# Kernel optimization log

Measured on AMD Instinct MI355X. Metric: run time of the kernel, lower is better.

The kernel has to match this reference:

```python
import jax, jax.numpy as jnp
import numpy as np

B, L, H = 4, 1024, 1024
NH, HD = 16, 64
ND = NH * HD
ITERS = 4
U = 5  # MSA1 ring window size (hard-coded in source)


def _conv1x1(w, b, x):  # w [O,C], b [O], x [B,C,L] -> [B,O,L]  (Conv2d 1x1 == per-position linear)
    return jnp.einsum('oc,bcl->bol', w, x) + b[None, :, None]


def _layernorm(x, s, b, eps=1e-5):  # x [B,H,L]; LayerNorm over channel dim H
    mu = x.mean(1, keepdims=True)
    var = ((x - mu) ** 2).mean(1, keepdims=True)
    return (x - mu) / jnp.sqrt(var + eps) * s[None, :, None] + b[None, :, None]


def _msa1(x, ax, wq, bq, wk, bk, wv, bv, wo, bo):
    # x [B,H,L] normalized nodes; ax [B,H,2,L] (ring embedding + relay)
    b, h, l = x.shape
    q = _conv1x1(wq, bq, x).reshape(b, NH, HD, l)
    k = _conv1x1(wk, bk, x).reshape(b, NH, HD, l)
    v = _conv1x1(wv, bv, x).reshape(b, NH, HD, l)
    pad = U // 2
    kp = jnp.pad(k, ((0, 0), (0, 0), (0, 0), (pad, pad)))
    vp = jnp.pad(v, ((0, 0), (0, 0), (0, 0), (pad, pad)))
    # F.unfold with (U,1) kernel along L == stack of U shifted views
    kw = jnp.stack([kp[..., u:u + l] for u in range(U)], axis=3)  # [B,NH,HD,U,L]
    vw = jnp.stack([vp[..., u:u + l] for u in range(U)], axis=3)
    al = ax.shape[2]
    ak = (jnp.einsum('oc,bcal->boal', wk, ax) + bk[None, :, None, None]).reshape(b, NH, HD, al, l)
    av = (jnp.einsum('oc,bcal->boal', wv, ax) + bv[None, :, None, None]).reshape(b, NH, HD, al, l)
    kw = jnp.concatenate([kw, ak], axis=3)  # [B,NH,HD,U+2,L]
    vw = jnp.concatenate([vw, av], axis=3)
    scores = (q[:, :, :, None, :] * kw).sum(2) / np.sqrt(HD)  # [B,NH,U+2,L]
    alphas = jax.nn.softmax(scores, axis=2)
    att = (alphas[:, :, None, :, :] * vw).sum(3).reshape(b, ND, l)
    return _conv1x1(wo, bo, att)  # [B,H,L]


def _msa2(relay, y, smask, wq, bq, wk, bk, wo, bo):
    # relay [B,H]; y [B,H,L+1]; smask [B,L+1] True at padding
    b = relay.shape[0]
    q = (jnp.einsum('oc,bc->bo', wq, relay) + bq).reshape(b, NH, HD)
    k = _conv1x1(wk, bk, y).reshape(b, NH, HD, -1)
    pre = jnp.einsum('bnd,bndl->bnl', q, k) / np.sqrt(HD)
    pre = jnp.where(smask[:, None, :], -1e10, pre)
    alphas = jax.nn.softmax(pre, axis=-1)
    # NOTE: source has v = k (WV output unused) -- reproduced faithfully
    att = jnp.einsum('bnl,bndl->bnd', alphas, k).reshape(b, ND)
    return jnp.einsum('oc,bc->bo', wo, att) + bo  # [B,H]


def _star_forward(data, mask, ln_s, ln_b, rwq, rwq_b, rwk, rwk_b, rwv, rwv_b, rwo, rwo_b,
                  swq, swq_b, swk, swk_b, swo, swo_b):
    b, l, h = data.shape
    pad_mask = (mask == 0)  # True at padding positions
    smask = jnp.concatenate([jnp.zeros((b, 1), bool), pad_mask], axis=1)  # [B,L+1]
    embs = jnp.transpose(data, (0, 2, 1))  # [B,H,L]
    nodes = embs
    relay = embs.mean(2)  # [B,H]
    for i in range(ITERS):
        xn = _layernorm(nodes, ln_s[i], ln_b[i])
        ax = jnp.stack([embs, jnp.broadcast_to(relay[:, :, None], embs.shape)], axis=2)  # [B,H,2,L]
        ring = _msa1(xn, ax, rwq[i], rwq_b[i], rwk[i], rwk_b[i], rwv[i], rwv_b[i], rwo[i], rwo_b[i])
        nodes = nodes + jax.nn.leaky_relu(ring)
        y = jnp.concatenate([relay[:, :, None], nodes], axis=2)  # [B,H,L+1]
        relay = jax.nn.leaky_relu(_msa2(relay, y, smask, swq[i], swq_b[i], swk[i], swk_b[i], swo[i], swo_b[i]))
        nodes = jnp.where(pad_mask[:, None, :], 0.0, nodes)
    return jnp.transpose(nodes, (0, 2, 1)), relay  # [B,L,H], [B,H]


def setup_inputs() -> dict:
    key = jax.random.key(0)
    ks = jax.random.split(key, 16)
    def p(k, shape):
        return jax.random.normal(k, shape, jnp.float32) * 0.02
    return dict(
        data=jax.random.normal(ks[0], (B, L, H), jnp.float32),
        mask=jax.random.randint(ks[1], (B, L), 0, 2).astype(jnp.int32),
        ln_s=jnp.ones((ITERS, H), jnp.float32),
        ln_b=jnp.zeros((ITERS, H), jnp.float32),
        rwq=p(ks[2], (ITERS, ND, H)), rwq_b=p(ks[3], (ITERS, ND)),
        rwk=p(ks[4], (ITERS, ND, H)), rwk_b=p(ks[5], (ITERS, ND)),
        rwv=p(ks[6], (ITERS, ND, H)), rwv_b=p(ks[7], (ITERS, ND)),
        rwo=p(ks[8], (ITERS, H, ND)), rwo_b=p(ks[9], (ITERS, H)),
        swq=p(ks[10], (ITERS, ND, H)), swq_b=p(ks[11], (ITERS, ND)),
        swk=p(ks[12], (ITERS, ND, H)), swk_b=p(ks[13], (ITERS, ND)),
        swo=p(ks[14], (ITERS, H, ND)), swo_b=p(ks[15], (ITERS, H)),
    )


def reference(data, mask, ln_s, ln_b, rwq, rwq_b, rwk, rwk_b, rwv, rwv_b, rwo, rwo_b,
              swq, swq_b, swk, swk_b, swo, swo_b):
    return _star_forward(data, mask, ln_s, ln_b, rwq, rwq_b, rwk, rwk_b, rwv, rwv_b,
                         rwo, rwo_b, swq, swq_b, swk, swk_b, swo, swo_b)
```

## Files before the change

### kernel.cpp

```cpp
#include <hip/hip_runtime.h>
#include <math.h>

namespace {

constexpr int B_ = 4, L_ = 1024, H_ = 1024, NH_ = 16, HD_ = 64, ND_ = 1024, ITERS_ = 4;

typedef unsigned short u16;
typedef __attribute__((ext_vector_type(8))) short short8;
typedef __attribute__((ext_vector_type(4))) float f32x4;

__device__ inline u16 f2bf(float f) {
  unsigned u = __builtin_bit_cast(unsigned, f);
  u += 0x7FFFu + ((u >> 16) & 1u);
  return (u16)(u >> 16);
}
__device__ inline float bf2f(u16 v) {
  unsigned u = ((unsigned)v) << 16;
  return __builtin_bit_cast(float, u);
}

__device__ inline void gl_lds16(const u16* g, u16* l) {
  __builtin_amdgcn_global_load_lds((const __attribute__((address_space(1))) void*)g,
                                   (__attribute__((address_space(3))) void*)l, 16, 0, 0);
}

__global__ void k_prep(const float* __restrict__ data, const float* __restrict__ rwq,
                       const float* __restrict__ rwk, const float* __restrict__ rwv,
                       const float* __restrict__ rwo, const float* __restrict__ swk,
                       u16* __restrict__ embs_bf, u16* __restrict__ wq_bf,
                       u16* __restrict__ wk_bf, u16* __restrict__ wv_bf,
                       u16* __restrict__ wo_bf, u16* __restrict__ swk_bf,
                       float* __restrict__ nodes) {
  int i = blockIdx.x * 256 + threadIdx.x;
  int which = blockIdx.y;
  if (which == 6) {
    reinterpret_cast<float4*>(nodes)[i] = reinterpret_cast<const float4*>(data)[i];
    return;
  }
  const float* src;
  u16* dst;
  switch (which) {
    case 0: src = data; dst = embs_bf; break;
    case 1: src = rwq; dst = wq_bf; break;
    case 2: src = rwk; dst = wk_bf; break;
    case 3: src = rwv; dst = wv_bf; break;
    case 4: src = rwo; dst = wo_bf; break;
    default: src = swk; dst = swk_bf; break;
  }
  float4 v = reinterpret_cast<const float4*>(src)[i];
  ushort4 o;
  o.x = f2bf(v.x); o.y = f2bf(v.y); o.z = f2bf(v.z); o.w = f2bf(v.w);
  reinterpret_cast<ushort4*>(dst)[i] = o;
}

__global__ void k_relay_part(const float* __restrict__ data, float* __restrict__ part) {
  int b = blockIdx.z, chunk = blockIdx.y;
  int c = blockIdx.x * 256 + threadIdx.x;
  const float* p = data + ((size_t)b * L_ + chunk * 128) * H_ + c;
  float acc = 0.f;
  for (int l = 0; l < 128; ++l) acc += p[(size_t)l * H_];
  part[((size_t)b * 8 + chunk) * H_ + c] = acc;
}
__global__ void k_relay_reduce(const float* __restrict__ part, float* __restrict__ relay) {
  int i = blockIdx.x * 256 + threadIdx.x;
  int b = i >> 10, c = i & 1023;
  float acc = 0.f;
  for (int j = 0; j < 8; ++j) acc += part[((size_t)b * 8 + j) * H_ + c];
  relay[i] = acc * (1.f / (float)L_);
}

__global__ __launch_bounds__(256) void k_layernorm_bf(float* __restrict__ nodes,
                                                      const float* __restrict__ s,
                                                      const float* __restrict__ bb,
                                                      const int* __restrict__ mask,
                                                      u16* __restrict__ y, int do_zero) {
  int row = blockIdx.x * 4 + (threadIdx.x >> 6);
  int lane = threadIdx.x & 63;
  int b = row >> 10, l = row & 1023;
  bool pad = do_zero && (mask[b * L_ + l] == 0);
  float4* xr = reinterpret_cast<float4*>(nodes + (size_t)row * H_);
  float4 v[4];
  float sum = 0.f, sq = 0.f;
#pragma unroll
  for (int j = 0; j < 4; ++j) {
    v[j] = pad ? float4{0.f, 0.f, 0.f, 0.f} : xr[lane + 64 * j];
    sum += v[j].x + v[j].y + v[j].z + v[j].w;
    sq += v[j].x * v[j].x + v[j].y * v[j].y + v[j].z * v[j].z + v[j].w * v[j].w;
  }
  if (pad) {
#pragma unroll
    for (int j = 0; j < 4; ++j) xr[lane + 64 * j] = float4{0.f, 0.f, 0.f, 0.f};
  }
#pragma unroll
  for (int off = 32; off; off >>= 1) {
    sum += __shfl_xor(sum, off);
    sq += __shfl_xor(sq, off);
  }
  float mu = sum * (1.f / (float)H_);
  float rstd = rsqrtf(sq * (1.f / (float)H_) - mu * mu + 1e-5f);
  ushort4* yr = reinterpret_cast<ushort4*>(y + (size_t)row * H_);
#pragma unroll
  for (int j = 0; j < 4; ++j) {
    int c4 = lane + 64 * j;
    float4 sc = reinterpret_cast<const float4*>(s)[c4];
    float4 bc = reinterpret_cast<const float4*>(bb)[c4];
    ushort4 o;
    o.x = f2bf((v[j].x - mu) * rstd * sc.x + bc.x);
    o.y = f2bf((v[j].y - mu) * rstd * sc.y + bc.y);
    o.z = f2bf((v[j].z - mu) * rstd * sc.z + bc.z);
    o.w = f2bf((v[j].w - mu) * rstd * sc.w + bc.w);
    yr[c4] = o;
  }
}


#define GEMM_PROLOGUE(XPTR, WPTR)                                              \
  __shared__ __align__(16) u16 sX[2][128 * 32];                                \
  __shared__ __align__(16) u16 sW[2][128 * 32];                                \
  const int t = threadIdx.x;                                                   \
  const int w = t >> 6, lane = t & 63;                                         \
  const int wm = w >> 1, wn = w & 1;                                           \
  const int r4 = lane >> 2, slot = lane & 3;                                   \
  const int rowS0 = w * 16 + r4, rowS1 = 64 + rowS0;                           \
  const int colS0 = ((slot ^ ((rowS0 >> 1) & 3)) << 3);                        \
  const int colS1 = ((slot ^ ((rowS1 >> 1) & 3)) << 3);                        \
  const u16* gX0 = (XPTR) + (size_t)(bm + rowS0) * 1024 + colS0;               \
  const u16* gX1 = (XPTR) + (size_t)(bm + rowS1) * 1024 + colS1;               \
  const u16* gW0 = (WPTR) + (size_t)(bn + rowS0) * 1024 + colS0;               \
  const u16* gW1 = (WPTR) + (size_t)(bn + rowS1) * 1024 + colS1;               \
  u16* lX0a = sX[0] + w * 512;                                                 \
  u16* lX0b = sX[1] + w * 512;                                                 \
  u16* lX1a = sX[0] + (4 + w) * 512;                                           \
  u16* lX1b = sX[1] + (4 + w) * 512;                                           \
  u16* lW0a = sW[0] + w * 512;                                                 \
  u16* lW0b = sW[1] + w * 512;                                                 \
  u16* lW1a = sW[0] + (4 + w) * 512;                                           \
  u16* lW1b = sW[1] + (4 + w) * 512;                                           \
  const int kidx = (((lane >> 4) ^ ((lane >> 1) & 3)) << 3);                   \
  f32x4 acc[4][4];                                                             \
  _Pragma("unroll") for (int i_ = 0; i_ < 4; ++i_)                             \
      _Pragma("unroll") for (int j_ = 0; j_ < 4; ++j_)                         \
          acc[i_][j_] = f32x4{0.f, 0.f, 0.f, 0.f};

#define GEMM_KLOOP64(AROWBASE, BROWBASE, ASRC, BSRC)                           \
  for (int ck = 0; ck < 1024; ck += 64) {                                      \
    gl_lds16(gX0, lX0a);                                                       \
    gl_lds16(gX0 + 32, lX0b);                                                  \
    gl_lds16(gX1, lX1a);                                                       \
    gl_lds16(gX1 + 32, lX1b);                                                  \
    gl_lds16(gW0, lW0a);                                                       \
    gl_lds16(gW0 + 32, lW0b);                                                  \
    gl_lds16(gW1, lW1a);                                                       \
    gl_lds16(gW1 + 32, lW1b);                                                  \
    gX0 += 64; gX1 += 64; gW0 += 64; gW1 += 64;                                \
    __syncthreads();                                                           \
    _Pragma("unroll") for (int h = 0; h < 2; ++h) {                            \
      short8 af_[4], bf_[4];                                                   \
      _Pragma("unroll") for (int mf = 0; mf < 4; ++mf)                         \
          af_[mf] = *reinterpret_cast<const short8*>(                          \
              &ASRC[h][((AROWBASE) + mf * 16) * 32 + kidx]);                   \
      _Pragma("unroll") for (int nf = 0; nf < 4; ++nf)                         \
          bf_[nf] = *reinterpret_cast<const short8*>(                          \
              &BSRC[h][((BROWBASE) + nf * 16) * 32 + kidx]);                   \
      _Pragma("unroll") for (int mf = 0; mf < 4; ++mf)                         \
          _Pragma("unroll") for (int nf = 0; nf < 4; ++nf)                     \
              acc[mf][nf] = __builtin_amdgcn_mfma_f32_16x16x32_bf16(           \
                  af_[mf], bf_[nf], acc[mf][nf], 0, 0, 0);                     \
    }                                                                          \
    __syncthreads();                                                          \
  }

__global__ __launch_bounds__(256, 3) void k_gemm5(const u16* __restrict__ wq,
                                                  const u16* __restrict__ wk,
                                                  const u16* __restrict__ wv,
                                                  const float* __restrict__ bq,
                                                  const float* __restrict__ bk,
                                                  const float* __restrict__ bv,
                                                  const u16* __restrict__ xn,
                                                  const u16* __restrict__ embs,
                                                  u16* __restrict__ Y) {
  const int bm = blockIdx.x * 128;
  const int which = blockIdx.y >> 3;
  const int bn = (blockIdx.y & 7) * 128;
  const u16* W = (which == 0) ? wq : ((which == 1 || which == 3) ? wk : wv);
  const float* bias = (which == 0) ? bq : ((which == 1 || which == 3) ? bk : bv);
  const u16* X = (which < 3) ? xn : embs;
  u16* Yw = Y + (size_t)which * ((size_t)B_ * L_ * ND_);

  GEMM_PROLOGUE(X, W)
  const int rW = wm * 64 + (lane & 15);
  const int rX = wn * 64 + (lane & 15);
  GEMM_KLOOP64(rW, rX, sW, sX)

#pragma unroll
  for (int mo = 0; mo < 4; ++mo) {
    int o0 = bn + wm * 64 + mo * 16 + ((lane >> 4) << 2);
    float4 bs = *reinterpret_cast<const float4*>(bias + o0);
#pragma unroll
    for (int nl = 0; nl < 4; ++nl) {
      int bl = bm + wn * 64 + nl * 16 + (lane & 15);
      f32x4 vv = acc[mo][nl];
      ushort4 ov;
      ov.x = f2bf(vv[0] + bs.x);
      ov.y = f2bf(vv[1] + bs.y);
      ov.z = f2bf(vv[2] + bs.z);
      ov.w = f2bf(vv[3] + bs.w);
      *reinterpret_cast<ushort4*>(&Yw[(size_t)bl * 1024 + o0]) = ov;
    }
  }
}


#define SMALL_PROLOGUE(XPTR, WPTR)                                             \
  __shared__ __align__(16) u16 sX[2][128 * 32];                                \
  __shared__ __align__(16) u16 sW[2][64 * 32];                                 \
  const int t = threadIdx.x;                                                   \
  const int w = t >> 6, lane = t & 63;                                         \
  const int wm = w >> 1, wn = w & 1;                                           \
  const int r4 = lane >> 2, slot = lane & 3;                                   \
  const int rowS0 = w * 16 + r4, rowS1 = 64 + rowS0;                           \
  const int colS0 = ((slot ^ ((rowS0 >> 1) & 3)) << 3);                        \
  const int colS1 = ((slot ^ ((rowS1 >> 1) & 3)) << 3);                        \
  const u16* gX0 = (XPTR) + (size_t)(bm + rowS0) * 1024 + colS0;               \
  const u16* gX1 = (XPTR) + (size_t)(bm + rowS1) * 1024 + colS1;               \
  const u16* gW0 = (WPTR) + (size_t)(bn + rowS0) * 1024 + colS0;               \
  u16* lX0a = sX[0] + w * 512;                                                 \
  u16* lX0b = sX[1] + w * 512;                                                 \
  u16* lX1a = sX[0] + (4 + w) * 512;                                           \
  u16* lX1b = sX[1] + (4 + w) * 512;                                           \
  u16* lW0a = sW[0] + w * 512;                                                 \
  u16* lW0b = sW[1] + w * 512;                                                 \
  const int kidx = (((lane >> 4) ^ ((lane >> 1) & 3)) << 3);

#define SMALL_KLOOP(MFN, NFN, ACC, AROWBASE, BROWBASE, ASRC, BSRC)             \
  for (int ck = 0; ck < 1024; ck += 64) {                                      \
    gl_lds16(gX0, lX0a);                                                       \
    gl_lds16(gX0 + 32, lX0b);                                                  \
    gl_lds16(gX1, lX1a);                                                       \
    gl_lds16(gX1 + 32, lX1b);                                                  \
    gl_lds16(gW0, lW0a);                                                       \
    gl_lds16(gW0 + 32, lW0b);                                                  \
    gX0 += 64; gX1 += 64; gW0 += 64;                                           \
    __syncthreads();                                                           \
    _Pragma("unroll") for (int h = 0; h < 2; ++h) {                            \
      short8 af_[MFN], bf_[NFN];                                               \
      _Pragma("unroll") for (int mf = 0; mf < MFN; ++mf)                       \
          af_[mf] = *reinterpret_cast<const short8*>(                          \
              &ASRC[h][((AROWBASE) + mf * 16) * 32 + kidx]);                   \
      _Pragma("unroll") for (int nf = 0; nf < NFN; ++nf)                       \
          bf_[nf] = *reinterpret_cast<const short8*>(                          \
              &BSRC[h][((BROWBASE) + nf * 16) * 32 + kidx]);                   \
      _Pragma("unroll") for (int mf = 0; mf < MFN; ++mf)                       \
          _Pragma("unroll") for (int nf = 0; nf < NFN; ++nf)                   \
              ACC[mf][nf] = __builtin_amdgcn_mfma_f32_16x16x32_bf16(           \
                  af_[mf], bf_[nf], ACC[mf][nf], 0, 0, 0);                     \
    }                                                                          \
    __syncthreads();                                                          \
  }

__global__ __launch_bounds__(256, 2) void k_gemm_wo_s(const u16* __restrict__ W,
                                                      const float* __restrict__ bias,
                                                      const u16* __restrict__ X,
                                                      float* __restrict__ nodes,
                                                      u16* __restrict__ nodes_bf) {
  const int bm = blockIdx.x * 128;
  const int bn = blockIdx.y * 64;
  SMALL_PROLOGUE(X, W)
  f32x4 acc[2][4];
#pragma unroll
  for (int i_ = 0; i_ < 2; ++i_)
#pragma unroll
    for (int j_ = 0; j_ < 4; ++j_) acc[i_][j_] = f32x4{0.f, 0.f, 0.f, 0.f};
  const int rW = wm * 32 + (lane & 15);
  const int rX = wn * 64 + (lane & 15);
  SMALL_KLOOP(2, 4, acc, rW, rX, sW, sX)

#pragma unroll
  for (int mo = 0; mo < 2; ++mo) {
    int o0 = bn + wm * 32 + mo * 16 + ((lane >> 4) << 2);
    float4 bs = *reinterpret_cast<const float4*>(bias + o0);
#pragma unroll
    for (int nl = 0; nl < 4; ++nl) {
      int bl = bm + wn * 64 + nl * 16 + (lane & 15);
      size_t ni = (size_t)bl * 1024 + o0;
      float4 curv = *reinterpret_cast<const float4*>(&nodes[ni]);
      f32x4 vv = acc[mo][nl];
      float r0 = vv[0] + bs.x; r0 = curv.x + (r0 > 0.f ? r0 : 0.01f * r0);
      float r1 = vv[1] + bs.y; r1 = curv.y + (r1 > 0.f ? r1 : 0.01f * r1);
      float r2 = vv[2] + bs.z; r2 = curv.z + (r2 > 0.f ? r2 : 0.01f * r2);
      float r3 = vv[3] + bs.w; r3 = curv.w + (r3 > 0.f ? r3 : 0.01f * r3);
      *reinterpret_cast<float4*>(&nodes[ni]) = float4{r0, r1, r2, r3};
      ushort4 ov;
      ov.x = f2bf(r0); ov.y = f2bf(r1); ov.z = f2bf(r2); ov.w = f2bf(r3);
      *reinterpret_cast<ushort4*>(&nodes_bf[ni]) = ov;
    }
  }
}

__global__ __launch_bounds__(256, 2) void k_gemm_kkb_sw(const u16* __restrict__ W,
                                                        const float* __restrict__ bias,
                                                        const u16* __restrict__ X,
                                                        u16* __restrict__ Y) {
  const int bm = blockIdx.x * 128;
  const int bn = blockIdx.y * 64;
  SMALL_PROLOGUE(X, W)
  f32x4 acc[2][4];
#pragma unroll
  for (int i_ = 0; i_ < 2; ++i_)
#pragma unroll
    for (int j_ = 0; j_ < 4; ++j_) acc[i_][j_] = f32x4{0.f, 0.f, 0.f, 0.f};
  const int rW = wm * 32 + (lane & 15);
  const int rX = wn * 64 + (lane & 15);
  SMALL_KLOOP(2, 4, acc, rW, rX, sW, sX)

#pragma unroll
  for (int mo = 0; mo < 2; ++mo) {
    int o0 = bn + wm * 32 + mo * 16 + ((lane >> 4) << 2);
    float4 bs = *reinterpret_cast<const float4*>(bias + o0);
#pragma unroll
    for (int nl = 0; nl < 4; ++nl) {
      int bl = bm + wn * 64 + nl * 16 + (lane & 15);
      size_t row = (size_t)(bl >> 10) * 1025 + 1 + (bl & 1023);
      f32x4 vv = acc[mo][nl];
      ushort4 ov;
      ov.x = f2bf(vv[0] + bs.x);
      ov.y = f2bf(vv[1] + bs.y);
      ov.z = f2bf(vv[2] + bs.z);
      ov.w = f2bf(vv[3] + bs.w);
      *reinterpret_cast<ushort4*>(&Y[row * 1024 + o0]) = ov;
    }
  }
}

__global__ __launch_bounds__(256) void k_matvec4(const float* __restrict__ W0,
                                                 const float* __restrict__ b0, float* __restrict__ y0,
                                                 const float* __restrict__ W1,
                                                 const float* __restrict__ b1, float* __restrict__ y1,
                                                 const float* __restrict__ W2,
                                                 const float* __restrict__ b2, float* __restrict__ y2,
                                                 const float* __restrict__ W3,
                                                 const float* __restrict__ b3, u16* __restrict__ y3b,
                                                 const float* __restrict__ x) {
  int b = blockIdx.y, z = blockIdx.z;
  const float* W = (z == 0) ? W0 : (z == 1) ? W1 : (z == 2) ? W2 : W3;
  const float* bias = (z == 0) ? b0 : (z == 1) ? b1 : (z == 2) ? b2 : b3;
  int o = blockIdx.x * 4 + (threadIdx.x >> 6);
  int lane = threadIdx.x & 63;
  const float* wr = W + (size_t)o * 1024;
  const float* xb = x + (size_t)b * 1024;
  float acc = 0.f;
  for (int c = lane; c < 1024; c += 64) acc += wr[c] * xb[c];
#pragma unroll
  for (int off = 32; off; off >>= 1) acc += __shfl_xor(acc, off);
  if (lane == 0) {
    acc += bias[o];
    if (z == 3) y3b[(size_t)b * 1025 * 1024 + o] = f2bf(acc);
    else if (z == 2) y2[(size_t)b * 1024 + o] = acc;
    else if (z == 1) y1[(size_t)b * 1024 + o] = acc;
    else y0[(size_t)b * 1024 + o] = acc;
  }
}

__global__ __launch_bounds__(256) void k_matvec(const float* __restrict__ W,
                                                const float* __restrict__ bias,
                                                const float* __restrict__ x,
                                                float* __restrict__ y, int leaky) {
  int b = blockIdx.y;
  int o = blockIdx.x * 4 + (threadIdx.x >> 6);
  int lane = threadIdx.x & 63;
  const float* wr = W + (size_t)o * 1024;
  const float* xb = x + (size_t)b * 1024;
  float acc = 0.f;
  for (int c = lane; c < 1024; c += 64) acc += wr[c] * xb[c];
#pragma unroll
  for (int off = 32; off; off >>= 1) acc += __shfl_xor(acc, off);
  if (lane == 0) {
    acc += bias[o];
    if (leaky) acc = acc > 0.f ? acc : 0.01f * acc;
    y[(size_t)b * 1024 + o] = acc;
  }
}

__global__ __launch_bounds__(256) void k_msa1(const u16* __restrict__ q,
                                              const u16* __restrict__ k,
                                              const u16* __restrict__ v,
                                              const u16* __restrict__ ke,
                                              const u16* __restrict__ ve,
                                              const float* __restrict__ rk,
                                              const float* __restrict__ rv,
                                              u16* __restrict__ attbf) {
  int t = threadIdx.x;
  int wv = t >> 6, lane = t & 63;
  int head = lane >> 2, dq = lane & 3;
  int l = blockIdx.x * 4 + wv;
  int b = blockIdx.z;
  size_t row = ((size_t)(b * 1024 + l)) * 1024 + head * 64 + dq * 16;
  size_t rbase = (size_t)b * 1024 + head * 64 + dq * 16;

  float qf[16];
  {
    const short8* qp = reinterpret_cast<const short8*>(q + row);
#pragma unroll
    for (int j = 0; j < 2; ++j) {
      short8 qv = qp[j];
#pragma unroll
      for (int e = 0; e < 8; ++e) qf[j * 8 + e] = bf2f((u16)qv[e]);
    }
  }
  float s[7];
#pragma unroll
  for (int u = 0; u < 5; ++u) {
    int lk = l + u - 2;
    float su = 0.f;
    if (lk >= 0 && lk < L_) {
      const short8* kp = reinterpret_cast<const short8*>(
          k + ((size_t)(b * 1024 + lk)) * 1024 + head * 64 + dq * 16);
#pragma unroll
      for (int j = 0; j < 2; ++j) {
        short8 kv = kp[j];
#pragma unroll
        for (int e = 0; e < 8; ++e) su = fmaf(qf[j * 8 + e], bf2f((u16)kv[e]), su);
      }
    }
    s[u] = su;
  }
  {
    float su = 0.f;
    const short8* kp = reinterpret_cast<const short8*>(ke + row);
#pragma unroll
    for (int j = 0; j < 2; ++j) {
      short8 kv = kp[j];
#pragma unroll
      for (int e = 0; e < 8; ++e) su = fmaf(qf[j * 8 + e], bf2f((u16)kv[e]), su);
    }
    s[5] = su;
  }
  {
    float su = 0.f;
    const float4* rp = reinterpret_cast<const float4*>(rk + rbase);
#pragma unroll
    for (int j = 0; j < 4; ++j) {
      float4 r4 = rp[j];
      su = fmaf(qf[j * 4 + 0], r4.x, su);
      su = fmaf(qf[j * 4 + 1], r4.y, su);
      su = fmaf(qf[j * 4 + 2], r4.z, su);
      su = fmaf(qf[j * 4 + 3], r4.w, su);
    }
    s[6] = su;
  }
#pragma unroll
  for (int u = 0; u < 7; ++u) {
    s[u] += __shfl_xor(s[u], 1);
    s[u] += __shfl_xor(s[u], 2);
  }
  float m = -1e30f;
#pragma unroll
  for (int u = 0; u < 7; ++u) {
    s[u] *= 0.125f;
    m = fmaxf(m, s[u]);
  }
  float e[7], tot = 0.f;
#pragma unroll
  for (int u = 0; u < 7; ++u) {
    e[u] = expf(s[u] - m);
    tot += e[u];
  }
  float inv = 1.f / tot;
#pragma unroll
  for (int u = 0; u < 7; ++u) e[u] *= inv;

  float av[16];
  {
    const float4* rp = reinterpret_cast<const float4*>(rv + rbase);
#pragma unroll
    for (int j = 0; j < 4; ++j) {
      float4 r4 = rp[j];
      av[j * 4 + 0] = e[6] * r4.x;
      av[j * 4 + 1] = e[6] * r4.y;
      av[j * 4 + 2] = e[6] * r4.z;
      av[j * 4 + 3] = e[6] * r4.w;
    }
  }
  {
    const short8* vp = reinterpret_cast<const short8*>(ve + row);
#pragma unroll
    for (int j = 0; j < 2; ++j) {
      short8 vvv = vp[j];
#pragma unroll
      for (int ee = 0; ee < 8; ++ee) av[j * 8 + ee] = fmaf(e[5], bf2f((u16)vvv[ee]), av[j * 8 + ee]);
    }
  }
#pragma unroll
  for (int u = 0; u < 5; ++u) {
    int lk = l + u - 2;
    if (lk >= 0 && lk < L_) {
      const short8* vp = reinterpret_cast<const short8*>(
          v + ((size_t)(b * 1024 + lk)) * 1024 + head * 64 + dq * 16);
#pragma unroll
      for (int j = 0; j < 2; ++j) {
        short8 vvv = vp[j];
#pragma unroll
        for (int ee = 0; ee < 8; ++ee) av[j * 8 + ee] = fmaf(e[u], bf2f((u16)vvv[ee]), av[j * 8 + ee]);
      }
    }
  }
  u16 ob[16];
#pragma unroll
  for (int j = 0; j < 16; ++j) ob[j] = f2bf(av[j]);
  uint4* d4 = reinterpret_cast<uint4*>(attbf + row);
  const uint4* s4 = reinterpret_cast<const uint4*>(ob);
  d4[0] = s4[0];
  d4[1] = s4[1];
}

__global__ __launch_bounds__(256) void k_msa2f(const u16* __restrict__ kkb,
                                               const float* __restrict__ rq,
                                               const int* __restrict__ mask,
                                               float* __restrict__ avp,
                                               float* __restrict__ Ep) {
  int b = blockIdx.y;
  int w = threadIdx.x >> 6, lane = threadIdx.x & 63;
  int wc = blockIdx.x * 4 + w;
  int q4 = lane & 3;
  int ch0 = lane * 16;
  float rqv[16];
  {
    const float4* rp = reinterpret_cast<const float4*>(rq + (size_t)b * 1024 + ch0);
#pragma unroll
    for (int j = 0; j < 4; ++j) {
      float4 v4 = rp[j];
      rqv[j * 4 + 0] = v4.x; rqv[j * 4 + 1] = v4.y;
      rqv[j * 4 + 2] = v4.z; rqv[j * 4 + 3] = v4.w;
    }
  }
  float av[16];
#pragma unroll
  for (int j = 0; j < 16; ++j) av[j] = 0.f;
  float eacc = 0.f;
  int p0 = wc * 16;
  int pend = p0 + 16;
  if (pend > 1025) pend = 1025;
  for (int p = p0; p < pend; ++p) {
    if (p > 0 && mask[b * L_ + p - 1] == 0) continue;
    const uint4* kr = reinterpret_cast<const uint4*>(kkb + ((size_t)b * 1025 + p) * 1024 + ch0);
    uint4 ka = kr[0], kb2 = kr[1];
    float kf[16];
    const u16* kp = reinterpret_cast<const u16*>(&ka);
#pragma unroll
    for (int j = 0; j < 8; ++j) kf[j] = bf2f(kp[j]);
    const u16* kp2 = reinterpret_cast<const u16*>(&kb2);
#pragma unroll
    for (int j = 0; j < 8; ++j) kf[8 + j] = bf2f(kp2[j]);
    float s = 0.f;
#pragma unroll
    for (int j = 0; j < 16; ++j) s = fmaf(rqv[j], kf[j], s);
    s += __shfl_xor(s, 1);
    s += __shfl_xor(s, 2);
    float e = expf(s * 0.125f);
    if (q4 == 0) eacc += e;
#pragma unroll
    for (int j = 0; j < 16; ++j) av[j] = fmaf(e, kf[j], av[j]);
  }
  float* ap = avp + ((size_t)b * 68 + wc) * 1024 + ch0;
#pragma unroll
  for (int j = 0; j < 4; ++j)
    reinterpret_cast<float4*>(ap)[j] =
        float4{av[j * 4 + 0], av[j * 4 + 1], av[j * 4 + 2], av[j * 4 + 3]};
  if (q4 == 0) Ep[((size_t)b * 68 + wc) * 16 + (lane >> 2)] = eacc;
}

__global__ void k_msa2r(const float* __restrict__ avp, const float* __restrict__ Ep,
                        float* __restrict__ satt) {
  int b = blockIdx.y;
  int idx = blockIdx.x * 256 + threadIdx.x;
  int head = idx >> 6;
  float a = 0.f, E = 0.f;
  for (int k = 0; k < 68; ++k) a += avp[((size_t)b * 68 + k) * 1024 + idx];
  for (int k = 0; k < 68; ++k) E += Ep[((size_t)b * 68 + k) * 16 + head];
  satt[(size_t)b * 1024 + idx] = a / E;
}

__global__ void k_final(const float* __restrict__ nodes, const int* __restrict__ mask,
                        float* __restrict__ out) {
  int i = blockIdx.x * 256 + threadIdx.x;
  int row = i >> 8;
  int b = row >> 10, l = row & 1023;
  float4 v = (mask[b * L_ + l] == 0) ? float4{0.f, 0.f, 0.f, 0.f}
                                     : reinterpret_cast<const float4*>(nodes)[i];
  reinterpret_cast<float4*>(out)[i] = v;
}

__global__ void k_copy_relay(const float* __restrict__ relay, float* __restrict__ out) {
  int i = blockIdx.x * 256 + threadIdx.x;
  out[i] = relay[i];
}

}

extern "C" void kernel_launch(void* const* d_in, const int* in_sizes, int n_in,
                              void* d_out, int out_size, void* d_ws, size_t ws_size,
                              hipStream_t stream) {
  (void)in_sizes; (void)n_in; (void)out_size; (void)ws_size;
  const float* data = (const float*)d_in[0];
  const int* mask = (const int*)d_in[1];
  const float* ln_s = (const float*)d_in[2];
  const float* ln_b = (const float*)d_in[3];
  const float* rwq = (const float*)d_in[4];
  const float* rwq_b = (const float*)d_in[5];
  const float* rwk = (const float*)d_in[6];
  const float* rwk_b = (const float*)d_in[7];
  const float* rwv = (const float*)d_in[8];
  const float* rwv_b = (const float*)d_in[9];
  const float* rwo = (const float*)d_in[10];
  const float* rwo_b = (const float*)d_in[11];
  const float* swq = (const float*)d_in[12];
  const float* swq_b = (const float*)d_in[13];
  const float* swk = (const float*)d_in[14];
  const float* swk_b = (const float*)d_in[15];
  const float* swo = (const float*)d_in[16];
  const float* swo_b = (const float*)d_in[17];
  float* out = (float*)d_out;

  const size_t SZ = (size_t)B_ * ND_ * L_;
  float* f = (float*)d_ws;
  float* nodes = f; f += SZ;
  float* part = f; f += (size_t)B_ * 8 * H_;
  float* relay = f; f += B_ * H_;
  float* rk = f; f += B_ * ND_;
  float* rv = f; f += B_ * ND_;
  float* rq = f; f += B_ * ND_;
  float* satt = f; f += B_ * ND_;
  float* avp = f; f += (size_t)B_ * 68 * 1024;
  float* Ep = f; f += (size_t)B_ * 68 * 16;
  u16* u = (u16*)f;
  u16* xn_bf = u; u += SZ;
  u16* embs_bf = u; u += SZ;
  u16* att_bf = u; u += SZ;
  u16* nodes_bf = u; u += SZ;
  u16* kkb_sw = u; u += (size_t)B_ * 1025 * 1024;
  u16* qkv5_bf = u; u += 5 * SZ;
  u16* wq_bf = u; u += SZ;
  u16* wk_bf = u; u += SZ;
  u16* wv_bf = u; u += SZ;
  u16* wo_bf = u; u += SZ;
  u16* swk_bf = u; u += SZ;

  k_prep<<<dim3(4096, 7), 256, 0, stream>>>(data, rwq, rwk, rwv, rwo, swk,
                                            embs_bf, wq_bf, wk_bf, wv_bf, wo_bf, swk_bf, nodes);
  k_relay_part<<<dim3(H_ / 256, 8, B_), 256, 0, stream>>>(data, part);
  k_relay_reduce<<<dim3((B_ * H_) / 256), 256, 0, stream>>>(part, relay);

  for (int i = 0; i < ITERS_; ++i) {
    const u16* wq_i = wq_bf + (size_t)i * ND_ * H_;
    const u16* wk_i = wk_bf + (size_t)i * ND_ * H_;
    const u16* wv_i = wv_bf + (size_t)i * ND_ * H_;
    const u16* wo_i = wo_bf + (size_t)i * H_ * ND_;
    const u16* sk_i = swk_bf + (size_t)i * ND_ * H_;

    k_layernorm_bf<<<dim3(B_ * L_ / 4), 256, 0, stream>>>(nodes, ln_s + i * H_, ln_b + i * H_,
                                                          mask, xn_bf, i > 0 ? 1 : 0);
    k_matvec4<<<dim3(256, B_, 4), 256, 0, stream>>>(
        rwk + (size_t)i * ND_ * H_, rwk_b + i * ND_, rk,
        rwv + (size_t)i * ND_ * H_, rwv_b + i * ND_, rv,
        swq + (size_t)i * ND_ * H_, swq_b + i * ND_, rq,
        swk + (size_t)i * ND_ * H_, swk_b + i * ND_, kkb_sw, relay);
    k_gemm5<<<dim3(32, 40), 256, 0, stream>>>(wq_i, wk_i, wv_i,
                                              rwq_b + i * ND_, rwk_b + i * ND_, rwv_b + i * ND_,
                                              xn_bf, embs_bf, qkv5_bf);
    k_msa1<<<dim3(L_ / 4, 1, B_), 256, 0, stream>>>(qkv5_bf, qkv5_bf + SZ, qkv5_bf + 2 * SZ,
                                                    qkv5_bf + 3 * SZ, qkv5_bf + 4 * SZ, rk, rv, att_bf);
    k_gemm_wo_s<<<dim3(32, 16), 256, 0, stream>>>(wo_i, rwo_b + i * H_, att_bf, nodes, nodes_bf);
    k_gemm_kkb_sw<<<dim3(32, 16), 256, 0, stream>>>(sk_i, swk_b + i * ND_, nodes_bf, kkb_sw);
    k_msa2f<<<dim3(17, B_), 256, 0, stream>>>(kkb_sw, rq, mask, avp, Ep);
    k_msa2r<<<dim3(4, B_), 256, 0, stream>>>(avp, Ep, satt);
    k_matvec<<<dim3(256, B_), 256, 0, stream>>>(swo + (size_t)i * H_ * ND_, swo_b + i * H_,
                                                satt, relay, 1);
  }
  k_final<<<4096, 256, 0, stream>>>(nodes, mask, out);
  k_copy_relay<<<dim3((B_ * H_) / 256), 256, 0, stream>>>(relay, out + (size_t)B_ * L_ * H_);
}
```

Measured before the change: 618.0 us.

## Software-pipeline GEMM K-loops with ping-pong LDS buffers and MFMA priority

Replaces the load-then-sync-then-compute K-loops in the projection GEMMs with a two-phase ping-pong schedule. Each phase issues direct global-to-LDS loads for the next 32-wide K slice into one buffer while running MFMAs on the other. A single vmcnt wait plus barrier replaces the two __syncthreads per iteration. MFMA sections are wrapped in s_setprio to favour matrix issue. The intent is to hide global load latency behind compute, at the cost of finer-grained barriers (one per 32-wide K slice rather than one per 64) and reliance on the buffer-reuse ordering being correct.

```diff
diff --git a/kernel.cpp b/kernel.cpp
--- a/kernel.cpp
+++ b/kernel.cpp
@@ -128,47 +128,55 @@
   const u16* gX1 = (XPTR) + (size_t)(bm + rowS1) * 1024 + colS1;               \
   const u16* gW0 = (WPTR) + (size_t)(bn + rowS0) * 1024 + colS0;               \
   const u16* gW1 = (WPTR) + (size_t)(bn + rowS1) * 1024 + colS1;               \
-  u16* lX0a = sX[0] + w * 512;                                                 \
-  u16* lX0b = sX[1] + w * 512;                                                 \
-  u16* lX1a = sX[0] + (4 + w) * 512;                                           \
-  u16* lX1b = sX[1] + (4 + w) * 512;                                           \
-  u16* lW0a = sW[0] + w * 512;                                                 \
-  u16* lW0b = sW[1] + w * 512;                                                 \
-  u16* lW1a = sW[0] + (4 + w) * 512;                                           \
-  u16* lW1b = sW[1] + (4 + w) * 512;                                           \
   const int kidx = (((lane >> 4) ^ ((lane >> 1) & 3)) << 3);                   \
   f32x4 acc[4][4];                                                             \
   _Pragma("unroll") for (int i_ = 0; i_ < 4; ++i_)                             \
       _Pragma("unroll") for (int j_ = 0; j_ < 4; ++j_)                         \
           acc[i_][j_] = f32x4{0.f, 0.f, 0.f, 0.f};
 
-#define GEMM_KLOOP64(AROWBASE, BROWBASE, ASRC, BSRC)                           \
-  for (int ck = 0; ck < 1024; ck += 64) {                                      \
-    gl_lds16(gX0, lX0a);                                                       \
-    gl_lds16(gX0 + 32, lX0b);                                                  \
-    gl_lds16(gX1, lX1a);                                                       \
-    gl_lds16(gX1 + 32, lX1b);                                                  \
-    gl_lds16(gW0, lW0a);                                                       \
-    gl_lds16(gW0 + 32, lW0b);                                                  \
-    gl_lds16(gW1, lW1a);                                                       \
-    gl_lds16(gW1 + 32, lW1b);                                                  \
-    gX0 += 64; gX1 += 64; gW0 += 64; gW1 += 64;                                \
-    __syncthreads();                                                           \
-    _Pragma("unroll") for (int h = 0; h < 2; ++h) {                            \
-      short8 af_[4], bf_[4];                                                   \
-      _Pragma("unroll") for (int mf = 0; mf < 4; ++mf)                         \
-          af_[mf] = *reinterpret_cast<const short8*>(                          \
-              &ASRC[h][((AROWBASE) + mf * 16) * 32 + kidx]);                   \
-      _Pragma("unroll") for (int nf = 0; nf < 4; ++nf)                         \
-          bf_[nf] = *reinterpret_cast<const short8*>(                          \
-              &BSRC[h][((BROWBASE) + nf * 16) * 32 + kidx]);                   \
-      _Pragma("unroll") for (int mf = 0; mf < 4; ++mf)                         \
-          _Pragma("unroll") for (int nf = 0; nf < 4; ++nf)                     \
-              acc[mf][nf] = __builtin_amdgcn_mfma_f32_16x16x32_bf16(           \
-                  af_[mf], bf_[nf], acc[mf][nf], 0, 0, 0);                     \
-    }                                                                          \
-    __syncthreads();                                                          \
-  }
+#define STAGE4(BUF)                                                            \
+  gl_lds16(gX0, sX[BUF] + w * 512);                                            \
+  gl_lds16(gX1, sX[BUF] + (4 + w) * 512);                                      \
+  gl_lds16(gW0, sW[BUF] + w * 512);                                            \
+  gl_lds16(gW1, sW[BUF] + (4 + w) * 512);                                      \
+  gX0 += 32; gX1 += 32; gW0 += 32; gW1 += 32;
+
+#define COMPUTE4(BUF, AROWBASE, BROWBASE, ASRC, BSRC)                          \
+  {                                                                            \
+    short8 af_[4], bf_[4];                                                     \
+    _Pragma("unroll") for (int mf = 0; mf < 4; ++mf)                           \
+        af_[mf] = *reinterpret_cast<const short8*>(                            \
+            &ASRC[BUF][((AROWBASE) + mf * 16) * 32 + kidx]);                   \
+    _Pragma("unroll") for (int nf = 0; nf < 4; ++nf)                           \
+        bf_[nf] = *reinterpret_cast<const short8*>(                            \
+            &BSRC[BUF][((BROWBASE) + nf * 16) * 32 + kidx]);                   \
+    __builtin_amdgcn_s_setprio(1);                                             \
+    _Pragma("unroll") for (int mf = 0; mf < 4; ++mf)                           \
+        _Pragma("unroll") for (int nf = 0; nf < 4; ++nf)                       \
+            acc[mf][nf] = __builtin_amdgcn_mfma_f32_16x16x32_bf16(             \
+                af_[mf], bf_[nf], acc[mf][nf], 0, 0, 0);                       \
+    __builtin_amdgcn_s_setprio(0);                                             \
+  }
+
+#define VMBAR                                                                  \
+  asm volatile("s_waitcnt vmcnt(0)" ::: "memory");                             \
+  __builtin_amdgcn_s_barrier();
+
+#define GEMM_KLOOP_2PH(AROWBASE, BROWBASE, ASRC, BSRC)                         \
+  STAGE4(0)                                                                    \
+  VMBAR                                                                        \
+  for (int tp = 0; tp < 15; ++tp) {                                            \
+    STAGE4(1)                                                                  \
+    COMPUTE4(0, AROWBASE, BROWBASE, ASRC, BSRC)                                \
+    VMBAR                                                                      \
+    STAGE4(0)                                                                  \
+    COMPUTE4(1, AROWBASE, BROWBASE, ASRC, BSRC)                                \
+    VMBAR                                                                      \
+  }                                                                            \
+  STAGE4(1)                                                                    \
+  COMPUTE4(0, AROWBASE, BROWBASE, ASRC, BSRC)                                  \
+  VMBAR                                                                        \
+  COMPUTE4(1, AROWBASE, BROWBASE, ASRC, BSRC)
 
 __global__ __launch_bounds__(256, 3) void k_gemm5(const u16* __restrict__ wq,
                                                   const u16* __restrict__ wk,
@@ -190,7 +198,7 @@
   GEMM_PROLOGUE(X, W)
   const int rW = wm * 64 + (lane & 15);
   const int rX = wn * 64 + (lane & 15);
-  GEMM_KLOOP64(rW, rX, sW, sX)
+  GEMM_KLOOP_2PH(rW, rX, sW, sX)
 
 #pragma unroll
   for (int mo = 0; mo < 4; ++mo) {
@@ -224,39 +232,50 @@
   const u16* gX0 = (XPTR) + (size_t)(bm + rowS0) * 1024 + colS0;               \
   const u16* gX1 = (XPTR) + (size_t)(bm + rowS1) * 1024 + colS1;               \
   const u16* gW0 = (WPTR) + (size_t)(bn + rowS0) * 1024 + colS0;               \
-  u16* lX0a = sX[0] + w * 512;                                                 \
-  u16* lX0b = sX[1] + w * 512;                                                 \
-  u16* lX1a = sX[0] + (4 + w) * 512;                                           \
-  u16* lX1b = sX[1] + (4 + w) * 512;                                           \
-  u16* lW0a = sW[0] + w * 512;                                                 \
-  u16* lW0b = sW[1] + w * 512;                                                 \
-  const int kidx = (((lane >> 4) ^ ((lane >> 1) & 3)) << 3);
-
-#define SMALL_KLOOP(MFN, NFN, ACC, AROWBASE, BROWBASE, ASRC, BSRC)             \
-  for (int ck = 0; ck < 1024; ck += 64) {                                      \
-    gl_lds16(gX0, lX0a);                                                       \
-    gl_lds16(gX0 + 32, lX0b);                                                  \
-    gl_lds16(gX1, lX1a);                                                       \
-    gl_lds16(gX1 + 32, lX1b);                                                  \
-    gl_lds16(gW0, lW0a);                                                       \
-    gl_lds16(gW0 + 32, lW0b);                                                  \
-    gX0 += 64; gX1 += 64; gW0 += 64;                                           \
-    __syncthreads();                                                           \
-    _Pragma("unroll") for (int h = 0; h < 2; ++h) {                            \
-      short8 af_[MFN], bf_[NFN];                                               \
-      _Pragma("unroll") for (int mf = 0; mf < MFN; ++mf)                       \
-          af_[mf] = *reinterpret_cast<const short8*>(                          \
-              &ASRC[h][((AROWBASE) + mf * 16) * 32 + kidx]);                   \
-      _Pragma("unroll") for (int nf = 0; nf < NFN; ++nf)                       \
-          bf_[nf] = *reinterpret_cast<const short8*>(                          \
-              &BSRC[h][((BROWBASE) + nf * 16) * 32 + kidx]);                   \
-      _Pragma("unroll") for (int mf = 0; mf < MFN; ++mf)                       \
-          _Pragma("unroll") for (int nf = 0; nf < NFN; ++nf)                   \
-              ACC[mf][nf] = __builtin_amdgcn_mfma_f32_16x16x32_bf16(           \
-                  af_[mf], bf_[nf], ACC[mf][nf], 0, 0, 0);                     \
-    }                                                                          \
-    __syncthreads();                                                          \
-  }
+  const int kidx = (((lane >> 4) ^ ((lane >> 1) & 3)) << 3);                   \
+  f32x4 acc[2][4];                                                             \
+  _Pragma("unroll") for (int i_ = 0; i_ < 2; ++i_)                             \
+      _Pragma("unroll") for (int j_ = 0; j_ < 4; ++j_)                         \
+          acc[i_][j_] = f32x4{0.f, 0.f, 0.f, 0.f};
+
+#define STAGE3(BUF)                                                            \
+  gl_lds16(gX0, sX[BUF] + w * 512);                                            \
+  gl_lds16(gX1, sX[BUF] + (4 + w) * 512);                                      \
+  gl_lds16(gW0, sW[BUF] + w * 512);                                            \
+  gX0 += 32; gX1 += 32; gW0 += 32;
+
+#define COMPUTE2x4(BUF, AROWBASE, BROWBASE, ASRC, BSRC)                        \
+  {                                                                            \
+    short8 af_[2], bf_[4];                                                     \
+    _Pragma("unroll") for (int mf = 0; mf < 2; ++mf)                           \
+        af_[mf] = *reinterpret_cast<const short8*>(                            \
+            &ASRC[BUF][((AROWBASE) + mf * 16) * 32 + kidx]);                   \
+    _Pragma("unroll") for (int nf = 0; nf < 4; ++nf)                           \
+        bf_[nf] = *reinterpret_cast<const short8*>(                            \
+            &BSRC[BUF][((BROWBASE) + nf * 16) * 32 + kidx]);                   \
+    __builtin_amdgcn_s_setprio(1);                                             \
+    _Pragma("unroll") for (int mf = 0; mf < 2; ++mf)                           \
+        _Pragma("unroll") for (int nf = 0; nf < 4; ++nf)                       \
+            acc[mf][nf] = __builtin_amdgcn_mfma_f32_16x16x32_bf16(             \
+                af_[mf], bf_[nf], acc[mf][nf], 0, 0, 0);                       \
+    __builtin_amdgcn_s_setprio(0);                                             \
+  }
+
+#define SMALL_KLOOP_2PH(AROWBASE, BROWBASE, ASRC, BSRC)                        \
+  STAGE3(0)                                                                    \
+  VMBAR                                                                        \
+  for (int tp = 0; tp < 15; ++tp) {                                            \
+    STAGE3(1)                                                                  \
+    COMPUTE2x4(0, AROWBASE, BROWBASE, ASRC, BSRC)                              \
+    VMBAR                                                                      \
+    STAGE3(0)                                                                  \
+    COMPUTE2x4(1, AROWBASE, BROWBASE, ASRC, BSRC)                              \
+    VMBAR                                                                      \
+  }                                                                            \
+  STAGE3(1)                                                                    \
+  COMPUTE2x4(0, AROWBASE, BROWBASE, ASRC, BSRC)                                \
+  VMBAR                                                                        \
+  COMPUTE2x4(1, AROWBASE, BROWBASE, ASRC, BSRC)
 
 __global__ __launch_bounds__(256, 2) void k_gemm_wo_s(const u16* __restrict__ W,
                                                       const float* __restrict__ bias,
@@ -266,14 +285,9 @@
   const int bm = blockIdx.x * 128;
   const int bn = blockIdx.y * 64;
   SMALL_PROLOGUE(X, W)
-  f32x4 acc[2][4];
-#pragma unroll
-  for (int i_ = 0; i_ < 2; ++i_)
-#pragma unroll
-    for (int j_ = 0; j_ < 4; ++j_) acc[i_][j_] = f32x4{0.f, 0.f, 0.f, 0.f};
   const int rW = wm * 32 + (lane & 15);
   const int rX = wn * 64 + (lane & 15);
-  SMALL_KLOOP(2, 4, acc, rW, rX, sW, sX)
+  SMALL_KLOOP_2PH(rW, rX, sW, sX)
 
 #pragma unroll
   for (int mo = 0; mo < 2; ++mo) {
@@ -304,14 +318,9 @@
   const int bm = blockIdx.x * 128;
   const int bn = blockIdx.y * 64;
   SMALL_PROLOGUE(X, W)
-  f32x4 acc[2][4];
-#pragma unroll
-  for (int i_ = 0; i_ < 2; ++i_)
-#pragma unroll
-    for (int j_ = 0; j_ < 4; ++j_) acc[i_][j_] = f32x4{0.f, 0.f, 0.f, 0.f};
   const int rW = wm * 32 + (lane & 15);
   const int rX = wn * 64 + (lane & 15);
-  SMALL_KLOOP(2, 4, acc, rW, rX, sW, sX)
+  SMALL_KLOOP_2PH(rW, rX, sW, sX)
 
 #pragma unroll
   for (int mo = 0; mo < 2; ++mo) {
```

Result: slower. 671.2 us (+8.6%).
